# Kernel optimization log

Hardware: AMD Instinct MI355X
Metric: run time of the kernel (lower is better)

Reference implementation:

```python
import jax, jax.numpy as jnp
import numpy as np

# 24 directional shifts (dy, dx): out[h,w] = in[h-dy, w-dx], zero elsewhere.
SHIFTS = [(0,1),(0,-1),(1,0),(-1,0),(1,1),(-1,-1),(1,-1),(-1,1),
          (0,2),(0,-2),(2,0),(-2,0),(2,2),(-2,-2),(2,-2),(-2,2),
          (2,1),(1,2),(2,-1),(1,-2),(-2,1),(-1,2),(-2,-1),(-1,-2)]

def shift2d(xg, dy, dx):
    B, G, H, W = xg.shape
    pt, pb = max(dy,0), max(-dy,0)
    pl, pr = max(dx,0), max(-dx,0)
    xp = jnp.pad(xg, ((0,0),(0,0),(pt,pb),(pl,pr)))
    return xp[:, :, pb:pb+H, pr:pr+W]

def mul_shift(x4, gamma=1.0/24.0):
    B, C, H, W = x4.shape
    g = int(C * gamma)
    parts = [shift2d(x4[:, i*g:(i+1)*g], dy, dx) for i, (dy, dx) in enumerate(SHIFTS)]
    parts.append(x4[:, 24*g:])
    return jnp.concatenate(parts, axis=1)

def zigzag_indices(h, w, start='top-left', direction='horizontal'):
    if start == 'top-left':   row_start, col_start, row_step, col_step = 0, 0, 1, 1
    elif start == 'top-right': row_start, col_start, row_step, col_step = 0, w-1, 1, -1
    elif start == 'bottom-left': row_start, col_start, row_step, col_step = h-1, 0, -1, 1
    else:                     row_start, col_start, row_step, col_step = h-1, w-1, -1, -1
    idx = []
    for i in range(h):
        r = row_start + row_step * i
        if direction == 'horizontal':
            cols = range(w) if r % 2 == 0 else range(w-1, -1, -1)
            idx += [r * w + c for c in cols]
        else:
            cc = col_start + col_step * i
            rows = range(h) if cc % 2 == 0 else range(h-1, -1, -1)
            idx += [rr * w + cc for rr in rows]
    return np.asarray(idx, dtype=np.int32)

def wkv(w, u, k, v):
    """Numerically stable RWKV WKV recurrence. w,u:(C,) k,v:(B,T,C) -> (B,T,C)."""
    B, T, C = k.shape
    def step(carry, kv):
        p, q, o = carry
        kt, vt = kv
        no = jnp.maximum(o, u + kt)
        A = jnp.exp(o - no); Bc = jnp.exp(u + kt - no)
        y = (A * p + Bc * vt) / (A * q + Bc)
        no2 = jnp.maximum(w + o, kt)
        A2 = jnp.exp(w + o - no2); B2 = jnp.exp(kt - no2)
        return (A2 * p + B2 * vt, A2 * q + B2, no2), y
    init = (jnp.zeros((B, C), k.dtype), jnp.zeros((B, C), k.dtype),
            jnp.full((B, C), -1e38, k.dtype))
    _, ys = jax.lax.scan(step, init, (jnp.swapaxes(k, 0, 1), jnp.swapaxes(v, 0, 1)))
    return jnp.swapaxes(ys, 0, 1)

def setup_inputs() -> dict:
    key = jax.random.key(0)
    ks = jax.random.split(key, 8)
    B, H, W, C = 8, 64, 64, 768
    scale = 0.02
    return {
        'x': jax.random.normal(ks[0], (B, H*W, C), jnp.float32),
        'key_w': jax.random.normal(ks[1], (C, C), jnp.float32) * scale,
        'value_w': jax.random.normal(ks[2], (C, C), jnp.float32) * scale,
        'receptance_w': jax.random.normal(ks[3], (C, C), jnp.float32) * scale,
        'output_w': jax.random.normal(ks[4], (C, C), jnp.float32) * scale,
        'spatial_decay': jax.random.normal(ks[5], (2, C), jnp.float32),
        'spatial_first': jax.random.normal(ks[6], (2, C), jnp.float32),
        'h': H, 'w': W,
    }

def reference(x, key_w, value_w, receptance_w, output_w, spatial_decay, spatial_first, h, w):
    B, T, C = x.shape
    # layer_id=0 -> scheme ('top-left','horizontal')
    order = jnp.asarray(zigzag_indices(h, w, 'top-left', 'horizontal'))
    inv = jnp.argsort(order)
    # jit_func: mul_shift in (B,C,H,W), zigzag reorder along T, projections
    x4 = jnp.transpose(x.reshape(B, h, w, C), (0, 3, 1, 2))
    x4 = mul_shift(x4)
    xs = jnp.transpose(x4.reshape(B, C, T)[:, :, order], (0, 2, 1))  # (B,T,C)
    k = xs @ key_w.T
    v = xs @ value_w.T
    sr = jax.nn.sigmoid(xs @ receptance_w.T)
    # recurrence j=0
    v = wkv(spatial_decay[0] / T, spatial_first[0] / T, k, v)
    # recurrence j=1: zigzag-permute, WKV, inverse-permute (horizontal -> same grid)
    k2 = k[:, order]
    v2 = v[:, order]
    v2 = wkv(spatial_decay[1] / T, spatial_first[1] / T, k2, v2)
    v = v2[:, inv]
    return (sr * v) @ output_w.T
```

## Files before the change

kernel.cpp:

```cpp
#include <hip/hip_runtime.h>
#include <hip/hip_bf16.h>
#include <hip/hip_fp16.h>

#define T_SEQ 4096
#define CDIM  768
#define BDIM  8
#define MROWS (BDIM * T_SEQ)
#define NKVR  (3 * CDIM)
#define CHL   32
#define NCH   (T_SEQ / CHL)
#define BC    (BDIM * CDIM)

typedef __attribute__((ext_vector_type(8))) short   short8;
typedef __attribute__((ext_vector_type(4))) float   floatx4;
typedef unsigned short ushort_t;
typedef unsigned int   uint_t;
struct ushort4_t { ushort_t x, y, z, w; };

__device__ __forceinline__ ushort_t f2b(float f) {
    __hip_bfloat16 h = __float2bfloat16(f);
    return *(ushort_t*)&h;
}
__device__ __forceinline__ float b2f(ushort_t s) {
    __hip_bfloat16 h;
    *(ushort_t*)&h = s;
    return __bfloat162float(h);
}
__device__ __forceinline__ ushort_t f2h(float f) {
    __half h = __float2half(f);
    return *(ushort_t*)&h;
}
__device__ __forceinline__ float h2f(ushort_t s) {
    __half h;
    *(ushort_t*)&h = s;
    return __half2float(h);
}

__device__ __forceinline__ void gload_lds16(const void* g, void* l) {
    __builtin_amdgcn_global_load_lds(
        (const __attribute__((address_space(1))) void*)g,
        (__attribute__((address_space(3))) void*)l, 16, 0, 0);
}

__constant__ int c_dy[24] = {0,0,1,-1,1,-1,1,-1,0,0,2,-2,2,-2,2,-2,2,1,2,1,-2,-1,-2,-1};
__constant__ int c_dx[24] = {1,-1,0,0,1,-1,-1,1,2,-2,0,0,2,-2,-2,2,1,2,-1,-2,1,2,-1,-2};

__global__ void cvt_weights(const float* __restrict__ kw, const float* __restrict__ vw,
                            const float* __restrict__ rw, const float* __restrict__ ow,
                            ushort_t* __restrict__ wkvr, ushort_t* __restrict__ wo) {
    int i = blockIdx.x * 256 + threadIdx.x;
    if (i < CDIM * CDIM) {
        wkvr[i]                   = f2b(kw[i]);
        wkvr[i + CDIM * CDIM]     = f2b(vw[i]);
        wkvr[i + 2 * CDIM * CDIM] = f2b(rw[i]);
        wo[i]                     = f2b(ow[i]);
    }
}

__global__ void shift_zigzag(const float* __restrict__ x, ushort_t* __restrict__ xs) {
    size_t i = (size_t)blockIdx.x * 256 + threadIdx.x;
    if (i >= (size_t)MROWS * (CDIM / 4)) return;
    int c4 = (int)(i % (CDIM / 4)) * 4;
    size_t bt = i / (CDIM / 4);
    int tz = (int)(bt % T_SEQ);
    int b  = (int)(bt / T_SEQ);
    int r = tz >> 6, pos = tz & 63;
    int xcol = (r & 1) ? (63 - pos) : pos;
    int g = c4 >> 5;
    int ys = r - c_dy[g];
    int xsrc = xcol - c_dx[g];
    float4 val = {0.f, 0.f, 0.f, 0.f};
    if ((unsigned)ys < 64u && (unsigned)xsrc < 64u)
        val = *(const float4*)(x + ((size_t)b * T_SEQ + (size_t)(ys * 64 + xsrc)) * CDIM + c4);
    ushort4_t o;
    o.x = f2b(val.x); o.y = f2b(val.y); o.z = f2b(val.z); o.w = f2b(val.w);
    *(ushort4_t*)(xs + bt * CDIM + c4) = o;
}

template <int MODE, int NB>
__global__ __launch_bounds__(256, 3) void gemm_bt(
    const ushort_t* __restrict__ A, const ushort_t* __restrict__ Bw,
    ushort_t* __restrict__ kvb, ushort_t* __restrict__ out_sr,
    float* __restrict__ out_f) {
    __shared__ ushort_t As[128 * 64];
    __shared__ ushort_t Bs[128 * 64];
    const int p    = blockIdx.x;
    const int xcd  = p & 7;
    const int s    = p >> 3;
    const int mb   = xcd + 8 * (s / NB);
    const int nb   = s % NB;
    const int m0   = mb * 128;
    const int n0   = nb * 128;
    const int t    = threadIdx.x;
    const int lane = t & 63;
    const int wv   = t >> 6;
    const int wm   = (wv & 1) * 64;
    const int wn   = (wv >> 1) * 64;
    const int srow = t >> 3;
    const int sch  = t & 7;
    const int l15  = lane & 15;
    const int l4   = lane >> 4;

    floatx4 acc[4][4];
#pragma unroll
    for (int i = 0; i < 4; i++)
#pragma unroll
        for (int j = 0; j < 4; j++) acc[i][j] = (floatx4){0.f, 0.f, 0.f, 0.f};

    for (int kk = 0; kk < CDIM; kk += 64) {
        __syncthreads();
#pragma unroll
        for (int j = 0; j < 4; j++) {
            const int rowA = 32 * j + srow;
            const int gc   = sch ^ (rowA & 7);
            gload_lds16(A  + (size_t)(m0 + rowA) * CDIM + kk + gc * 8,
                        (void*)(As + j * 2048 + t * 8));
            gload_lds16(Bw + (size_t)(n0 + rowA) * CDIM + kk + gc * 8,
                        (void*)(Bs + j * 2048 + t * 8));
        }
        __syncthreads();
#pragma unroll
        for (int k2 = 0; k2 < 2; k2++) {
            short8 af[4], bfv[4];
#pragma unroll
            for (int mi = 0; mi < 4; mi++) {
                int ra = wm + mi * 16 + l15;
                int c  = k2 * 4 + l4;
                af[mi] = *(const short8*)(As + ra * 64 + ((c ^ (ra & 7)) << 3));
            }
#pragma unroll
            for (int ni = 0; ni < 4; ni++) {
                int rb = wn + ni * 16 + l15;
                int c  = k2 * 4 + l4;
                bfv[ni] = *(const short8*)(Bs + rb * 64 + ((c ^ (rb & 7)) << 3));
            }
#pragma unroll
            for (int mi = 0; mi < 4; mi++)
#pragma unroll
                for (int ni = 0; ni < 4; ni++)
                    acc[mi][ni] = __builtin_amdgcn_mfma_f32_16x16x32_bf16(
                        af[mi], bfv[ni], acc[mi][ni], 0, 0, 0);
        }
    }

    const int region = (MODE == 0) ? (nb / 6) : 0;
    const int ncb = n0 - region * CDIM;
#pragma unroll
    for (int mi = 0; mi < 4; mi++) {
#pragma unroll
        for (int ni = 0; ni < 4; ni++) {
            int nc = ncb + wn + ni * 16 + l15;
#pragma unroll
            for (int r = 0; r < 4; r++) {
                int mg = m0 + wm + mi * 16 + l4 * 4 + r;
                float val = acc[mi][ni][r];
                if (MODE == 0) {
                    if (region == 0)
                        kvb[((size_t)mg * CDIM + nc) * 2] = f2h(val);
                    else if (region == 1)
                        kvb[((size_t)mg * CDIM + nc) * 2 + 1] = f2h(val);
                    else
                        out_sr[(size_t)mg * CDIM + nc] =
                            f2b(1.0f / (1.0f + __expf(-val)));
                } else {
                    out_f[(size_t)mg * CDIM + (n0 + wn + ni * 16 + l15)] = val;
                }
            }
        }
    }
}


__global__ __launch_bounds__(256) void wkv_chunk_sum0(
    const uint_t* __restrict__ kvbuf, const float* __restrict__ sd,
    float* __restrict__ sumP, float* __restrict__ sumQ, float* __restrict__ sumO) {
    int gid = blockIdx.x * 256 + threadIdx.x;
    int bc = gid % BC;
    int ch = gid / BC;
    int b = bc / CDIM, c = bc % CDIM;
    const float w = sd[c] * (1.0f / (float)T_SEQ);
    const uint_t* kv = kvbuf + ((size_t)b * T_SEQ + ch * CHL) * CDIM + c;
    float p = 0.f, q = 0.f, o = -1e38f;
#pragma unroll 8
    for (int i = 0; i < CHL; i++) {
        uint_t u = kv[(size_t)i * CDIM];
        float kt = h2f((ushort_t)(u & 0xffff)), vt = h2f((ushort_t)(u >> 16));
        float wo_ = w + o;
        float no2 = fmaxf(wo_, kt);
        float A2 = __expf(wo_ - no2), B2 = __expf(kt - no2);
        p = A2 * p + B2 * vt;
        q = A2 * q + B2;
        o = no2;
    }
    size_t idx = (size_t)ch * BC + bc;
    sumP[idx] = p; sumQ[idx] = q; sumO[idx] = o;
}

__global__ __launch_bounds__(256) void wkv_chunk_scan(
    const float* __restrict__ sumP, const float* __restrict__ sumQ,
    const float* __restrict__ sumO,
    float* __restrict__ inP, float* __restrict__ inQ, float* __restrict__ inO,
    const float* __restrict__ sd, int pass) {
    int bc = blockIdx.x * 256 + threadIdx.x;
    if (bc >= BC) return;
    int c = bc % CDIM;
    const float w = sd[pass * CDIM + c] * (1.0f / (float)T_SEQ);
    const float Lw = w * (float)CHL;
    float p = 0.f, q = 0.f, o = -1e38f;
    for (int ch = 0; ch < NCH; ch++) {
        size_t idx = (size_t)ch * BC + bc;
        inP[idx] = p; inQ[idx] = q; inO[idx] = o;
        float Pc = sumP[idx], Qc = sumQ[idx], Oc = sumO[idx];
        float ow_ = o + Lw;
        float no = fmaxf(ow_, Oc);
        float e1 = __expf(ow_ - no), e2 = __expf(Oc - no);
        p = e1 * p + e2 * Pc;
        q = e1 * q + e2 * Qc;
        o = no;
    }
}

__global__ __launch_bounds__(256) void wkv_replay0_sum1(
    uint_t* __restrict__ kvbuf,
    const float* __restrict__ sd, const float* __restrict__ sf,
    const float* __restrict__ inP, const float* __restrict__ inQ,
    const float* __restrict__ inO,
    float* __restrict__ sumP, float* __restrict__ sumQ, float* __restrict__ sumO) {
    int gid = blockIdx.x * 256 + threadIdx.x;
    int bc = gid % BC;
    int ch = gid / BC;
    int b = bc / CDIM, c = bc % CDIM;
    const float w1 = sd[c] * (1.0f / (float)T_SEQ);
    const float u1 = sf[c] * (1.0f / (float)T_SEQ);
    uint_t* kv = kvbuf + ((size_t)b * T_SEQ + ch * CHL) * CDIM + c;
    size_t idx = (size_t)ch * BC + bc;
    float p = inP[idx], q = inQ[idx], o = inO[idx];
    float yv[CHL];
    float kvk[CHL];
#pragma unroll
    for (int i = 0; i < CHL; i++) {
        uint_t u = kv[(size_t)i * CDIM];
        float kt = h2f((ushort_t)(u & 0xffff)), vt = h2f((ushort_t)(u >> 16));
        kvk[i] = kt;
        float uk = u1 + kt;
        float no = fmaxf(o, uk);
        float Ae = __expf(o - no), Be = __expf(uk - no);
        float y = (Ae * p + Be * vt) / (Ae * q + Be);
        float wo_ = w1 + o;
        float no2 = fmaxf(wo_, kt);
        float A2 = __expf(wo_ - no2), B2 = __expf(kt - no2);
        p = A2 * p + B2 * vt;
        q = A2 * q + B2;
        o = no2;
        yv[i] = y;
        ((ushort_t*)&kv[(size_t)i * CDIM])[1] = f2h(y);
    }
    const float w2 = sd[CDIM + c] * (1.0f / (float)T_SEQ);
    float p2 = 0.f, q2 = 0.f, o2 = -1e38f;
    const bool rev = (ch >> 1) & 1;
#pragma unroll
    for (int j = 0; j < CHL; j++) {
        int i = rev ? (CHL - 1 - j) : j;
        float kt = kvk[i], vt = yv[i];
        float wo_ = w2 + o2;
        float no2 = fmaxf(wo_, kt);
        float A2 = __expf(wo_ - no2), B2 = __expf(kt - no2);
        p2 = A2 * p2 + B2 * vt;
        q2 = A2 * q2 + B2;
        o2 = no2;
    }
    size_t idx2 = (size_t)((ch & 2) ? (ch ^ 1) : ch) * BC + bc;
    sumP[idx2] = p2; sumQ[idx2] = q2; sumO[idx2] = o2;
}

__global__ __launch_bounds__(256) void wkv_replay1(
    const uint_t* __restrict__ kvbuf,
    const ushort_t* __restrict__ srb, ushort_t* __restrict__ a2,
    const float* __restrict__ sd, const float* __restrict__ sf,
    const float* __restrict__ inP, const float* __restrict__ inQ,
    const float* __restrict__ inO) {
    int gid = blockIdx.x * 256 + threadIdx.x;
    int bc = gid % BC;
    int ch = gid / BC;
    int b = bc / CDIM, c = bc % CDIM;
    const float w = sd[CDIM + c] * (1.0f / (float)T_SEQ);
    const float u = sf[CDIM + c] * (1.0f / (float)T_SEQ);
    size_t base = (size_t)b * T_SEQ * CDIM + c;
    size_t idx = (size_t)ch * BC + bc;
    float p = inP[idx], q = inQ[idx], o = inO[idx];
    const int r = ch >> 1;
    const int pos0 = (ch & 1) * CHL;
#pragma unroll 8
    for (int i = 0; i < CHL; i++) {
        int pos = pos0 + i;
        int col = (r & 1) ? (63 - pos) : pos;
        size_t off = base + (size_t)(r * 64 + col) * CDIM;
        uint_t uu = kvbuf[off];
        float kt = h2f((ushort_t)(uu & 0xffff)), vt = h2f((ushort_t)(uu >> 16));
        float uk = u + kt;
        float no = fmaxf(o, uk);
        float Ae = __expf(o - no), Be = __expf(uk - no);
        float y = (Ae * p + Be * vt) / (Ae * q + Be);
        float wo_ = w + o;
        float no2 = fmaxf(wo_, kt);
        float A2 = __expf(wo_ - no2), B2 = __expf(kt - no2);
        p = A2 * p + B2 * vt;
        q = A2 * q + B2;
        o = no2;
        a2[off] = f2b(y * b2f(srb[off]));
    }
}

extern "C" void kernel_launch(void* const* d_in, const int* in_sizes, int n_in,
                              void* d_out, int out_size, void* d_ws, size_t ws_size,
                              hipStream_t stream) {
    (void)in_sizes; (void)n_in; (void)out_size; (void)ws_size;
    const float* x  = (const float*)d_in[0];
    const float* kw = (const float*)d_in[1];
    const float* vw = (const float*)d_in[2];
    const float* rw = (const float*)d_in[3];
    const float* ow = (const float*)d_in[4];
    const float* sd = (const float*)d_in[5];
    const float* sf = (const float*)d_in[6];
    float* out = (float*)d_out;

    char* ws = (char*)d_ws;
    size_t off = 0;
    auto alloc = [&](size_t bytes) -> void* {
        void* p = ws + off;
        off += (bytes + 255) & ~(size_t)255;
        return p;
    };
    ushort_t* xs   = (ushort_t*)alloc((size_t)MROWS * CDIM * 2);
    ushort_t* kvb  = (ushort_t*)alloc((size_t)MROWS * CDIM * 4);
    ushort_t* srb  = (ushort_t*)alloc((size_t)MROWS * CDIM * 2);
    ushort_t* wkvr = (ushort_t*)alloc((size_t)NKVR * CDIM * 2);
    ushort_t* wo   = (ushort_t*)alloc((size_t)CDIM * CDIM * 2);
    float*    sumP = (float*)   alloc((size_t)NCH * BC * 4);
    float*    sumQ = (float*)   alloc((size_t)NCH * BC * 4);
    float*    sumO = (float*)   alloc((size_t)NCH * BC * 4);
    float*    inP  = (float*)   alloc((size_t)NCH * BC * 4);
    float*    inQ  = (float*)   alloc((size_t)NCH * BC * 4);
    float*    inO  = (float*)   alloc((size_t)NCH * BC * 4);

    cvt_weights<<<(CDIM * CDIM + 255) / 256, 256, 0, stream>>>(kw, vw, rw, ow, wkvr, wo);
    shift_zigzag<<<(int)(((size_t)MROWS * (CDIM / 4) + 255) / 256), 256, 0, stream>>>(x, xs);
    gemm_bt<0, 18><<<(MROWS / 128) * (NKVR / 128), 256, 0, stream>>>(
        xs, wkvr, kvb, srb, nullptr);

    const int nwkv = NCH * BC;
    wkv_chunk_sum0<<<nwkv / 256, 256, 0, stream>>>((uint_t*)kvb, sd, sumP, sumQ, sumO);
    wkv_chunk_scan<<<(BC + 255) / 256, 256, 0, stream>>>(sumP, sumQ, sumO,
                                                         inP, inQ, inO, sd, 0);
    wkv_replay0_sum1<<<nwkv / 256, 256, 0, stream>>>((uint_t*)kvb, sd, sf,
                                                     inP, inQ, inO, sumP, sumQ, sumO);
    wkv_chunk_scan<<<(BC + 255) / 256, 256, 0, stream>>>(sumP, sumQ, sumO,
                                                         inP, inQ, inO, sd, 1);
    wkv_replay1<<<nwkv / 256, 256, 0, stream>>>((uint_t*)kvb, srb, xs,
                                                sd, sf, inP, inQ, inO);

    gemm_bt<1, 6><<<(MROWS / 128) * (CDIM / 128), 256, 0, stream>>>(
        xs, wo, nullptr, nullptr, out);
}
```

Measured before the change: 587.0 us.

## Rewrite GEMM as 256x256 tile double-buffered pipeline and split K/V buffers

The bf16 GEMM now uses 256x256 output tiles with 512 threads and a two-stage LDS double buffer. Global loads for the next k-tiles are interleaved between MFMA phases using explicit waitcnt, barriers and setprio, so loads overlap with compute instead of fully synchronising each k-step. The interleaved K/V half-precision buffer is split into separate K and V arrays, which gives contiguous 2-byte stores in the GEMM epilogue and plain loads in the WKV kernels. The trade-off is higher register and LDS use (128 KB LDS, 8x4 accumulators per wave) and fewer, larger blocks, which may hurt occupancy and tail balance.

```diff
diff --git a/kernel.cpp b/kernel.cpp
--- a/kernel.cpp
+++ b/kernel.cpp
@@ -10,6 +10,7 @@
 #define CHL   32
 #define NCH   (T_SEQ / CHL)
 #define BC    (BDIM * CDIM)
+#define NKT   (CDIM / 64)
 
 typedef __attribute__((ext_vector_type(8))) short   short8;
 typedef __attribute__((ext_vector_type(4))) float   floatx4;
@@ -77,93 +78,134 @@
     *(ushort4_t*)(xs + bt * CDIM + c4) = o;
 }
 
+
+__device__ __forceinline__ void stage_half(const ushort_t* __restrict__ G,
+                                           int grow0, int kk,
+                                           ushort_t* dst, int t) {
+#pragma unroll
+    for (int i = 0; i < 2; i++) {
+        const int ci = i * 512 + t;
+        const int r  = ci >> 3;
+        const int sx = ci & 7;
+        gload_lds16(G + (size_t)(grow0 + r) * CDIM + kk + ((sx ^ (r & 7)) << 3),
+                    (void*)(dst + ci * 8));
+    }
+}
+
+#define READ_A(MIBASE, K2)                                                  \
+    _Pragma("unroll")                                                       \
+    for (int j = 0; j < 4; j++) {                                           \
+        const int rra = ((MIBASE) + j) * 16 + l15;                          \
+        af[j] = *(const short8*)(aReg + rra * 64 +                          \
+                                 ((((K2) * 4 + l4) ^ (rra & 7)) << 3));     \
+    }
+
+#define PHASE_TAIL(MIBASE, K2)                                              \
+    __builtin_amdgcn_s_barrier();                                           \
+    asm volatile("s_waitcnt lgkmcnt(0)" ::: "memory");                      \
+    __builtin_amdgcn_sched_barrier(0);                                      \
+    __builtin_amdgcn_s_setprio(1);                                          \
+    _Pragma("unroll")                                                       \
+    for (int j = 0; j < 4; j++) {                                           \
+        _Pragma("unroll")                                                   \
+        for (int ni = 0; ni < 4; ni++)                                      \
+            acc[(MIBASE) + j][ni] = __builtin_amdgcn_mfma_f32_16x16x32_bf16(\
+                af[j], bf[ni][K2], acc[(MIBASE) + j][ni], 0, 0, 0);         \
+    }                                                                       \
+    __builtin_amdgcn_s_setprio(0);                                          \
+    __builtin_amdgcn_s_barrier();
+
 template <int MODE, int NB>
-__global__ __launch_bounds__(256, 3) void gemm_bt(
+__global__ __launch_bounds__(512, 2) void gemm_bt(
     const ushort_t* __restrict__ A, const ushort_t* __restrict__ Bw,
-    ushort_t* __restrict__ kvb, ushort_t* __restrict__ out_sr,
-    float* __restrict__ out_f) {
-    __shared__ ushort_t As[128 * 64];
-    __shared__ ushort_t Bs[128 * 64];
-    const int p    = blockIdx.x;
-    const int xcd  = p & 7;
-    const int s    = p >> 3;
-    const int mb   = xcd + 8 * (s / NB);
-    const int nb   = s % NB;
-    const int m0   = mb * 128;
-    const int n0   = nb * 128;
+    ushort_t* __restrict__ kbuf, ushort_t* __restrict__ vbuf,
+    ushort_t* __restrict__ out_sr, float* __restrict__ out_f) {
+    __shared__ ushort_t lds[2][4][128 * 64];
+    const int pid  = blockIdx.x;
+    const int xcd  = pid & 7;
+    const int sid  = pid >> 3;
+    const int mb   = xcd + 8 * (sid / NB);
+    const int nb   = sid % NB;
+    const int m0   = mb * 256;
+    const int n0   = nb * 256;
     const int t    = threadIdx.x;
     const int lane = t & 63;
     const int wv   = t >> 6;
-    const int wm   = (wv & 1) * 64;
-    const int wn   = (wv >> 1) * 64;
-    const int srow = t >> 3;
-    const int sch  = t & 7;
+    const int wr   = wv >> 2;
+    const int wn   = (wv & 3) * 64;
+    const int bRi  = 2 + (wn >> 7);
+    const int wn64 = wn & 64;
     const int l15  = lane & 15;
     const int l4   = lane >> 4;
 
-    floatx4 acc[4][4];
-#pragma unroll
-    for (int i = 0; i < 4; i++)
+    floatx4 acc[8][4];
+#pragma unroll
+    for (int i = 0; i < 8; i++)
 #pragma unroll
         for (int j = 0; j < 4; j++) acc[i][j] = (floatx4){0.f, 0.f, 0.f, 0.f};
 
-    for (int kk = 0; kk < CDIM; kk += 64) {
-        __syncthreads();
-#pragma unroll
-        for (int j = 0; j < 4; j++) {
-            const int rowA = 32 * j + srow;
-            const int gc   = sch ^ (rowA & 7);
-            gload_lds16(A  + (size_t)(m0 + rowA) * CDIM + kk + gc * 8,
-                        (void*)(As + j * 2048 + t * 8));
-            gload_lds16(Bw + (size_t)(n0 + rowA) * CDIM + kk + gc * 8,
-                        (void*)(Bs + j * 2048 + t * 8));
+    stage_half(Bw, n0,       0,  &lds[0][2][0], t);
+    stage_half(Bw, n0 + 128, 0,  &lds[0][3][0], t);
+    stage_half(A,  m0,       0,  &lds[0][0][0], t);
+    stage_half(A,  m0 + 128, 0,  &lds[0][1][0], t);
+    stage_half(Bw, n0,       64, &lds[1][2][0], t);
+    stage_half(Bw, n0 + 128, 64, &lds[1][3][0], t);
+    stage_half(A,  m0,       64, &lds[1][0][0], t);
+    asm volatile("s_waitcnt vmcnt(6)" ::: "memory");
+    __builtin_amdgcn_s_barrier();
+
+#pragma unroll 2
+    for (int kt = 0; kt < NKT; kt++) {
+        const int p  = kt & 1;
+        const int pn = p ^ 1;
+        const ushort_t* aReg = &lds[p][wr][0];
+        const ushort_t* bReg = &lds[p][bRi][0];
+        short8 af[4];
+        short8 bf[4][2];
+#pragma unroll
+        for (int ni = 0; ni < 4; ni++) {
+            const int rrb = wn64 + ni * 16 + l15;
+            const ushort_t* bp = bReg + rrb * 64;
+            bf[ni][0] = *(const short8*)(bp + ((l4       ^ (rrb & 7)) << 3));
+            bf[ni][1] = *(const short8*)(bp + (((4 + l4) ^ (rrb & 7)) << 3));
         }
-        __syncthreads();
-#pragma unroll
-        for (int k2 = 0; k2 < 2; k2++) {
-            short8 af[4], bfv[4];
-#pragma unroll
-            for (int mi = 0; mi < 4; mi++) {
-                int ra = wm + mi * 16 + l15;
-                int c  = k2 * 4 + l4;
-                af[mi] = *(const short8*)(As + ra * 64 + ((c ^ (ra & 7)) << 3));
-            }
-#pragma unroll
-            for (int ni = 0; ni < 4; ni++) {
-                int rb = wn + ni * 16 + l15;
-                int c  = k2 * 4 + l4;
-                bfv[ni] = *(const short8*)(Bs + rb * 64 + ((c ^ (rb & 7)) << 3));
-            }
-#pragma unroll
-            for (int mi = 0; mi < 4; mi++)
-#pragma unroll
-                for (int ni = 0; ni < 4; ni++)
-                    acc[mi][ni] = __builtin_amdgcn_mfma_f32_16x16x32_bf16(
-                        af[mi], bfv[ni], acc[mi][ni], 0, 0, 0);
-        }
-    }
-
-    const int region = (MODE == 0) ? (nb / 6) : 0;
+        READ_A(0, 0)
+        if (kt + 1 < NKT) stage_half(A, m0 + 128, (kt + 1) * 64, &lds[pn][1][0], t);
+        PHASE_TAIL(0, 0)
+        READ_A(4, 0)
+        if (kt + 2 < NKT) stage_half(Bw, n0, (kt + 2) * 64, &lds[p][2][0], t);
+        PHASE_TAIL(4, 0)
+        READ_A(0, 1)
+        if (kt + 2 < NKT) stage_half(Bw, n0 + 128, (kt + 2) * 64, &lds[p][3][0], t);
+        PHASE_TAIL(0, 1)
+        READ_A(4, 1)
+        if (kt + 2 < NKT) stage_half(A, m0, (kt + 2) * 64, &lds[p][0][0], t);
+        if (kt < NKT - 2) { asm volatile("s_waitcnt vmcnt(6)" ::: "memory"); }
+        else              { asm volatile("s_waitcnt vmcnt(0)" ::: "memory"); }
+        PHASE_TAIL(4, 1)
+    }
+
+    const int region = (MODE == 0) ? (nb / 3) : 0;
     const int ncb = n0 - region * CDIM;
 #pragma unroll
-    for (int mi = 0; mi < 4; mi++) {
+    for (int mi = 0; mi < 8; mi++) {
 #pragma unroll
         for (int ni = 0; ni < 4; ni++) {
-            int nc = ncb + wn + ni * 16 + l15;
+            const int nc = ncb + wn + ni * 16 + l15;
 #pragma unroll
             for (int r = 0; r < 4; r++) {
-                int mg = m0 + wm + mi * 16 + l4 * 4 + r;
+                const int mg = m0 + wr * 128 + mi * 16 + l4 * 4 + r;
                 float val = acc[mi][ni][r];
                 if (MODE == 0) {
                     if (region == 0)
-                        kvb[((size_t)mg * CDIM + nc) * 2] = f2h(val);
+                        kbuf[(size_t)mg * CDIM + nc] = f2h(val);
                     else if (region == 1)
-                        kvb[((size_t)mg * CDIM + nc) * 2 + 1] = f2h(val);
+                        vbuf[(size_t)mg * CDIM + nc] = f2h(val);
                     else
                         out_sr[(size_t)mg * CDIM + nc] =
                             f2b(1.0f / (1.0f + __expf(-val)));
                 } else {
-                    out_f[(size_t)mg * CDIM + (n0 + wn + ni * 16 + l15)] = val;
+                    out_f[(size_t)mg * CDIM + nc] = val;
                 }
             }
         }
@@ -172,19 +214,21 @@
 
 
 __global__ __launch_bounds__(256) void wkv_chunk_sum0(
-    const uint_t* __restrict__ kvbuf, const float* __restrict__ sd,
+    const ushort_t* __restrict__ kb, const ushort_t* __restrict__ vb,
+    const float* __restrict__ sd,
     float* __restrict__ sumP, float* __restrict__ sumQ, float* __restrict__ sumO) {
     int gid = blockIdx.x * 256 + threadIdx.x;
     int bc = gid % BC;
     int ch = gid / BC;
     int b = bc / CDIM, c = bc % CDIM;
     const float w = sd[c] * (1.0f / (float)T_SEQ);
-    const uint_t* kv = kvbuf + ((size_t)b * T_SEQ + ch * CHL) * CDIM + c;
+    const size_t base = ((size_t)b * T_SEQ + ch * CHL) * CDIM + c;
+    const ushort_t* kp = kb + base;
+    const ushort_t* vp = vb + base;
     float p = 0.f, q = 0.f, o = -1e38f;
 #pragma unroll 8
     for (int i = 0; i < CHL; i++) {
-        uint_t u = kv[(size_t)i * CDIM];
-        float kt = h2f((ushort_t)(u & 0xffff)), vt = h2f((ushort_t)(u >> 16));
+        float kt = h2f(kp[(size_t)i * CDIM]), vt = h2f(vp[(size_t)i * CDIM]);
         float wo_ = w + o;
         float no2 = fmaxf(wo_, kt);
         float A2 = __expf(wo_ - no2), B2 = __expf(kt - no2);
@@ -221,7 +265,7 @@
 }
 
 __global__ __launch_bounds__(256) void wkv_replay0_sum1(
-    uint_t* __restrict__ kvbuf,
+    const ushort_t* __restrict__ kb, ushort_t* __restrict__ vb,
     const float* __restrict__ sd, const float* __restrict__ sf,
     const float* __restrict__ inP, const float* __restrict__ inQ,
     const float* __restrict__ inO,
@@ -232,15 +276,16 @@
     int b = bc / CDIM, c = bc % CDIM;
     const float w1 = sd[c] * (1.0f / (float)T_SEQ);
     const float u1 = sf[c] * (1.0f / (float)T_SEQ);
-    uint_t* kv = kvbuf + ((size_t)b * T_SEQ + ch * CHL) * CDIM + c;
+    const size_t base = ((size_t)b * T_SEQ + ch * CHL) * CDIM + c;
+    const ushort_t* kp = kb + base;
+    ushort_t* vp = vb + base;
     size_t idx = (size_t)ch * BC + bc;
     float p = inP[idx], q = inQ[idx], o = inO[idx];
     float yv[CHL];
     float kvk[CHL];
 #pragma unroll
     for (int i = 0; i < CHL; i++) {
-        uint_t u = kv[(size_t)i * CDIM];
-        float kt = h2f((ushort_t)(u & 0xffff)), vt = h2f((ushort_t)(u >> 16));
+        float kt = h2f(kp[(size_t)i * CDIM]), vt = h2f(vp[(size_t)i * CDIM]);
         kvk[i] = kt;
         float uk = u1 + kt;
         float no = fmaxf(o, uk);
@@ -253,7 +298,7 @@
         q = A2 * q + B2;
         o = no2;
         yv[i] = y;
-        ((ushort_t*)&kv[(size_t)i * CDIM])[1] = f2h(y);
+        vp[(size_t)i * CDIM] = f2h(y);
     }
     const float w2 = sd[CDIM + c] * (1.0f / (float)T_SEQ);
     float p2 = 0.f, q2 = 0.f, o2 = -1e38f;
@@ -274,7 +319,7 @@
 }
 
 __global__ __launch_bounds__(256) void wkv_replay1(
-    const uint_t* __restrict__ kvbuf,
+    const ushort_t* __restrict__ kb, const ushort_t* __restrict__ vb,
     const ushort_t* __restrict__ srb, ushort_t* __restrict__ a2,
     const float* __restrict__ sd, const float* __restrict__ sf,
     const float* __restrict__ inP, const float* __restrict__ inQ,
@@ -295,8 +340,7 @@
         int pos = pos0 + i;
         int col = (r & 1) ? (63 - pos) : pos;
         size_t off = base + (size_t)(r * 64 + col) * CDIM;
-        uint_t uu = kvbuf[off];
-        float kt = h2f((ushort_t)(uu & 0xffff)), vt = h2f((ushort_t)(uu >> 16));
+        float kt = h2f(kb[off]), vt = h2f(vb[off]);
         float uk = u + kt;
         float no = fmaxf(o, uk);
         float Ae = __expf(o - no), Be = __expf(uk - no);
@@ -332,7 +376,8 @@
         return p;
     };
     ushort_t* xs   = (ushort_t*)alloc((size_t)MROWS * CDIM * 2);
-    ushort_t* kvb  = (ushort_t*)alloc((size_t)MROWS * CDIM * 4);
+    ushort_t* kb   = (ushort_t*)alloc((size_t)MROWS * CDIM * 2);
+    ushort_t* vb   = (ushort_t*)alloc((size_t)MROWS * CDIM * 2);
     ushort_t* srb  = (ushort_t*)alloc((size_t)MROWS * CDIM * 2);
     ushort_t* wkvr = (ushort_t*)alloc((size_t)NKVR * CDIM * 2);
     ushort_t* wo   = (ushort_t*)alloc((size_t)CDIM * CDIM * 2);
@@ -345,20 +390,20 @@
 
     cvt_weights<<<(CDIM * CDIM + 255) / 256, 256, 0, stream>>>(kw, vw, rw, ow, wkvr, wo);
     shift_zigzag<<<(int)(((size_t)MROWS * (CDIM / 4) + 255) / 256), 256, 0, stream>>>(x, xs);
-    gemm_bt<0, 18><<<(MROWS / 128) * (NKVR / 128), 256, 0, stream>>>(
-        xs, wkvr, kvb, srb, nullptr);
+    gemm_bt<0, 9><<<(MROWS / 256) * (NKVR / 256), 512, 0, stream>>>(
+        xs, wkvr, kb, vb, srb, nullptr);
 
     const int nwkv = NCH * BC;
-    wkv_chunk_sum0<<<nwkv / 256, 256, 0, stream>>>((uint_t*)kvb, sd, sumP, sumQ, sumO);
+    wkv_chunk_sum0<<<nwkv / 256, 256, 0, stream>>>(kb, vb, sd, sumP, sumQ, sumO);
     wkv_chunk_scan<<<(BC + 255) / 256, 256, 0, stream>>>(sumP, sumQ, sumO,
                                                          inP, inQ, inO, sd, 0);
-    wkv_replay0_sum1<<<nwkv / 256, 256, 0, stream>>>((uint_t*)kvb, sd, sf,
+    wkv_replay0_sum1<<<nwkv / 256, 256, 0, stream>>>(kb, vb, sd, sf,
                                                      inP, inQ, inO, sumP, sumQ, sumO);
     wkv_chunk_scan<<<(BC + 255) / 256, 256, 0, stream>>>(sumP, sumQ, sumO,
                                                          inP, inQ, inO, sd, 1);
-    wkv_replay1<<<nwkv / 256, 256, 0, stream>>>((uint_t*)kvb, srb, xs,
+    wkv_replay1<<<nwkv / 256, 256, 0, stream>>>(kb, vb, srb, xs,
                                                 sd, sf, inP, inQ, inO);
 
-    gemm_bt<1, 6><<<(MROWS / 128) * (CDIM / 128), 256, 0, stream>>>(
-        xs, wo, nullptr, nullptr, out);
-}
+    gemm_bt<1, 3><<<(MROWS / 256) * (CDIM / 256), 512, 0, stream>>>(
+        xs, wo, nullptr, nullptr, nullptr, out);
+}
```

Result: no change. 594.1 us (+1.2%).
